# Kernel tuning notes

Measured on AMD Instinct MI355X. Metric: run time of the kernel, lower is better.

The kernel has to match this reference:

```python
import jax, jax.numpy as jnp
import numpy as np

D_MODEL = 256
NUM_HEADS = 4
D_K = D_MODEL // NUM_HEADS
SCALE = float(np.sqrt(D_K))


def setup_inputs() -> dict:
    key = jax.random.key(0)
    ks = jax.random.split(key, 11)
    B, S, D = 8, 2048, D_MODEL
    inp = {
        "query": jax.random.normal(ks[0], (B, S, D), dtype=jnp.float32),
        "key": jax.random.normal(ks[1], (B, S, D), dtype=jnp.float32),
        "value": jax.random.normal(ks[2], (B, S, D), dtype=jnp.float32),
        "W_q": jax.random.normal(ks[3], (D, D), dtype=jnp.float32) / np.sqrt(D),
        "b_q": jnp.zeros((D,), dtype=jnp.float32),
        "W_k": jax.random.normal(ks[4], (D, D), dtype=jnp.float32) / np.sqrt(D),
        "b_k": jnp.zeros((D,), dtype=jnp.float32),
        "W_v": jax.random.normal(ks[5], (D, D), dtype=jnp.float32) / np.sqrt(D),
        "b_v": jnp.zeros((D,), dtype=jnp.float32),
        "W_o": jax.random.normal(ks[6], (D, D), dtype=jnp.float32) / np.sqrt(D),
        "b_o": jnp.zeros((D,), dtype=jnp.float32),
    }
    return inp


def reference(query, key, value, W_q, b_q, W_k, b_k, W_v, b_v, W_o, b_o):
    B, Sq, D = query.shape
    Sk = key.shape[1]
    H, dk = NUM_HEADS, D_K
    # projections (torch Linear equivalent: x @ W + b with W as (in,out))
    Q = (query @ W_q + b_q).reshape(B, Sq, H, dk).transpose(0, 2, 1, 3)  # (B,H,Sq,dk)
    K = (key @ W_k + b_k).reshape(B, Sk, H, dk).transpose(0, 2, 1, 3)    # (B,H,Sk,dk)
    V = value @ W_v + b_v                                                # (B,Sk,D) shared across heads
    scores = jnp.einsum("bhqd,bhkd->bhqk", Q, K) / SCALE                 # (B,H,Sq,Sk)
    attn = jax.nn.softmax(scores, axis=-1)
    avg_attn = attn.mean(axis=1)                                         # (B,Sq,Sk)
    out = jnp.einsum("bqk,bkd->bqd", avg_attn, V)
    out = out @ W_o + b_o
    return out, avg_attn
```

## Files before the change

kernel.cpp:

```cpp
#include <hip/hip_runtime.h>
#include <stdint.h>

#define S2048 2048
#define DMODEL 256
#define NH 4
#define DK 64

typedef __bf16 bf16x8 __attribute__((ext_vector_type(8)));
typedef float f32x4 __attribute__((ext_vector_type(4)));

#define MFMA16(a, b, c) __builtin_amdgcn_mfma_f32_16x16x32_bf16((a), (b), (c), 0, 0, 0)

__device__ __forceinline__ uint16_t f2bf(float f) {
  uint32_t u = __builtin_bit_cast(uint32_t, f);
  u = (u + 0x7fff + ((u >> 16) & 1)) >> 16;
  return (uint16_t)u;
}

__device__ __forceinline__ void async16(const void* g, void* l) {
  __builtin_amdgcn_global_load_lds(
      (const __attribute__((address_space(1))) unsigned int*)g,
      (__attribute__((address_space(3))) unsigned int*)l, 16, 0, 0);
}

__device__ __forceinline__ void stage64(const char* gbase, int rstride,
                                        char* lds, int tid, int rows) {
  int iters = rows >> 5;
#pragma unroll
  for (int it = 0; it < iters; ++it) {
    int cid = (it << 8) + tid;
    int m = cid >> 3, cp = cid & 7, c = cp ^ (m & 7);
    async16(gbase + (size_t)m * rstride + (c << 4),
            lds + ((size_t)((it << 8) + (tid & ~63)) << 4));
  }
}

__device__ __forceinline__ bf16x8 frag_ld(const char* t, int rowbase, int chunk, int l15) {
  int m = rowbase + l15;
  return *(const bf16x8*)(t + (((m << 3) + (chunk ^ (m & 7))) << 4));
}

__global__ __launch_bounds__(256) void cast_x(const float* __restrict__ q,
                                              const float* __restrict__ k,
                                              const float* __restrict__ v,
                                              uint16_t* __restrict__ xq,
                                              uint16_t* __restrict__ xk,
                                              uint16_t* __restrict__ xv) {
  const float* src = blockIdx.y == 0 ? q : (blockIdx.y == 1 ? k : v);
  uint16_t* dst = blockIdx.y == 0 ? xq : (blockIdx.y == 1 ? xk : xv);
  size_t i = ((size_t)blockIdx.x * 256 + threadIdx.x) * 8;
  float4 a = *(const float4*)(src + i);
  float4 b = *(const float4*)(src + i + 4);
  union { uint16_t s[8]; uint4 u; } r;
  r.s[0] = f2bf(a.x); r.s[1] = f2bf(a.y); r.s[2] = f2bf(a.z); r.s[3] = f2bf(a.w);
  r.s[4] = f2bf(b.x); r.s[5] = f2bf(b.y); r.s[6] = f2bf(b.z); r.s[7] = f2bf(b.w);
  *(uint4*)(dst + i) = r.u;
}

__global__ __launch_bounds__(256) void cast_w(const float* __restrict__ Wq,
                                              const float* __restrict__ Wk,
                                              const float* __restrict__ Wv,
                                              const float* __restrict__ Wo,
                                              uint16_t* __restrict__ Wqt,
                                              uint16_t* __restrict__ Wkt,
                                              uint16_t* __restrict__ Wvt,
                                              uint16_t* __restrict__ Wot) {
  const float* W = blockIdx.y == 0 ? Wq : blockIdx.y == 1 ? Wk : blockIdx.y == 2 ? Wv : Wo;
  uint16_t* Wt = blockIdx.y == 0 ? Wqt : blockIdx.y == 1 ? Wkt : blockIdx.y == 2 ? Wvt : Wot;
  __shared__ uint16_t t[64 * 66];
  int tile = blockIdx.x, tr = tile >> 2, tc = tile & 3;
  int tid = threadIdx.x;
#pragma unroll
  for (int i = 0; i < 16; ++i) {
    int e = i * 256 + tid, r = e >> 6, cl = e & 63;
    t[r * 66 + cl] = f2bf(W[(size_t)(tr * 64 + r) * 256 + tc * 64 + cl]);
  }
  __syncthreads();
#pragma unroll
  for (int i = 0; i < 16; ++i) {
    int e = i * 256 + tid, n = e >> 6, kk = e & 63;
    Wt[(size_t)(tc * 64 + n) * 256 + tr * 64 + kk] = t[kk * 66 + n];
  }
}

template <int OUTF32, int BIAS>
__global__ __launch_bounds__(256) void gemm_bt(const uint16_t* __restrict__ A,
                                               const uint16_t* __restrict__ Bt,
                                               const float* __restrict__ bias,
                                               void* __restrict__ Cv, int K, int ldc) {
  __shared__ char lds[32768];
  char* At = lds;
  char* Btl = lds + 16384;
  int tid = threadIdx.x, lane = tid & 63, wid = tid >> 6;
  int l15 = lane & 15, q = lane >> 4;
  int mt = blockIdx.x, nt = blockIdx.y;
  int wm = (wid >> 1) * 64, wn = (wid & 1) * 64;
  f32x4 acc[4][4] = {};
  const char* Ag = (const char*)(A + (size_t)(mt * 128) * K);
  const char* Bg = (const char*)(Bt + (size_t)(nt * 128) * K);
  int nk = K >> 6;
  for (int kt = 0; kt < nk; ++kt) {
    stage64(Ag + kt * 128, K * 2, At, tid, 128);
    stage64(Bg + kt * 128, K * 2, Btl, tid, 128);
    __syncthreads();
#pragma unroll
    for (int ks = 0; ks < 2; ++ks) {
      bf16x8 a[4], b[4];
#pragma unroll
      for (int i = 0; i < 4; ++i) a[i] = frag_ld(At, wm + i * 16, ks * 4 + q, l15);
#pragma unroll
      for (int j = 0; j < 4; ++j) b[j] = frag_ld(Btl, wn + j * 16, ks * 4 + q, l15);
#pragma unroll
      for (int i = 0; i < 4; ++i)
#pragma unroll
        for (int j = 0; j < 4; ++j) acc[i][j] = MFMA16(a[i], b[j], acc[i][j]);
    }
    __syncthreads();
  }
#pragma unroll
  for (int i = 0; i < 4; ++i) {
    int r0 = mt * 128 + wm + i * 16 + q * 4;
#pragma unroll
    for (int j = 0; j < 4; ++j) {
      int c = nt * 128 + wn + j * 16 + l15;
#pragma unroll
      for (int e = 0; e < 4; ++e) {
        float v = acc[i][j][e];
        if (BIAS == 1) v += bias[c];
        if (BIAS == 2) v += bias[r0 + e];
        size_t off = (size_t)(r0 + e) * ldc + c;
        if (OUTF32) ((float*)Cv)[off] = v;
        else ((uint16_t*)Cv)[off] = f2bf(v);
      }
    }
  }
}

__global__ __launch_bounds__(256) void attn_lsum(const uint16_t* __restrict__ Qb,
                                                 const uint16_t* __restrict__ Kb,
                                                 float* __restrict__ linv4) {
  __shared__ char lds[32768];
  char* Qt = lds;
  char* Kt = lds + 16384;
  int tid = threadIdx.x, lane = tid & 63, wid = tid >> 6;
  int l15 = lane & 15, q = lane >> 4;
  int b = blockIdx.z, h = blockIdx.y, qt = blockIdx.x;
  const char* Qg = (const char*)(Qb + ((size_t)b * S2048 + qt * 128) * DMODEL + h * DK);
  const char* Kg = (const char*)(Kb + ((size_t)b * S2048) * DMODEL + h * DK);
  stage64(Qg, DMODEL * 2, Qt, tid, 128);
  float ps[2][4] = {};
  for (int kt = 0; kt < 16; ++kt) {
    stage64(Kg + (size_t)kt * 128 * (DMODEL * 2), DMODEL * 2, Kt, tid, 128);
    __syncthreads();
#pragma unroll
    for (int i = 0; i < 2; ++i) {
      bf16x8 a0 = frag_ld(Qt, wid * 32 + i * 16, q, l15);
      bf16x8 a1 = frag_ld(Qt, wid * 32 + i * 16, 4 + q, l15);
#pragma unroll
      for (int j = 0; j < 8; ++j) {
        f32x4 s = {0.f, 0.f, 0.f, 0.f};
        s = MFMA16(a0, frag_ld(Kt, j * 16, q, l15), s);
        s = MFMA16(a1, frag_ld(Kt, j * 16, 4 + q, l15), s);
#pragma unroll
        for (int e = 0; e < 4; ++e) ps[i][e] += __expf(s[e] * 0.125f);
      }
    }
    __syncthreads();
  }
#pragma unroll
  for (int i = 0; i < 2; ++i)
#pragma unroll
    for (int e = 0; e < 4; ++e) {
      float v = ps[i][e];
      v += __shfl_xor(v, 1); v += __shfl_xor(v, 2);
      v += __shfl_xor(v, 4); v += __shfl_xor(v, 8);
      if (l15 == 0) {
        int row = qt * 128 + wid * 32 + i * 16 + q * 4 + e;
        linv4[((size_t)(b * NH + h)) * S2048 + row] = 0.25f / v;
      }
    }
}

__global__ __launch_bounds__(256) void attn_avg(const uint16_t* __restrict__ Qb,
                                                const uint16_t* __restrict__ Kb,
                                                const float* __restrict__ linv4,
                                                float* __restrict__ attn) {
  __shared__ char lds[65536];
  char* Qt = lds;
  int tid = threadIdx.x, lane = tid & 63, wid = tid >> 6;
  int l15 = lane & 15, q = lane >> 4;
  int b = blockIdx.z, qt = blockIdx.y, kslice = blockIdx.x;
  size_t qrow0 = (size_t)b * S2048 + qt * 64;
#pragma unroll
  for (int h = 0; h < NH; ++h)
    stage64((const char*)(Qb + qrow0 * DMODEL + h * DK), DMODEL * 2, Qt + h * 8192, tid, 64);
  float li[4][4];
#pragma unroll
  for (int h = 0; h < NH; ++h)
#pragma unroll
    for (int e = 0; e < 4; ++e)
      li[h][e] = linv4[((size_t)(b * NH + h)) * S2048 + qt * 64 + wid * 16 + q * 4 + e];
  const char* Kg = (const char*)(Kb + ((size_t)b * S2048 + kslice * 512) * DMODEL);
  stage64(Kg, DMODEL * 2, lds + 32768, tid, 128);
  f32x4 Pav[8] = {};
  __syncthreads();
  for (int s = 0; s < 16; ++s) {
    int kt = s >> 2, h = s & 3;
    if (s + 1 < 16) {
      int kt2 = (s + 1) >> 2, h2 = (s + 1) & 3;
      stage64(Kg + (size_t)kt2 * 128 * (DMODEL * 2) + h2 * 128, DMODEL * 2,
              lds + 32768 + (((s + 1) & 1) << 14), tid, 128);
    }
    const char* Kc = lds + 32768 + ((s & 1) << 14);
    const char* Qh = Qt + h * 8192;
    bf16x8 a0 = frag_ld(Qh, wid * 16, q, l15);
    bf16x8 a1 = frag_ld(Qh, wid * 16, 4 + q, l15);
#pragma unroll
    for (int j = 0; j < 8; ++j) {
      f32x4 sA = {0.f, 0.f, 0.f, 0.f};
      sA = MFMA16(a0, frag_ld(Kc, j * 16, q, l15), sA);
      sA = MFMA16(a1, frag_ld(Kc, j * 16, 4 + q, l15), sA);
#pragma unroll
      for (int e = 0; e < 4; ++e) Pav[j][e] += __expf(sA[e] * 0.125f) * li[h][e];
    }
    if (h == 3) {
      size_t rowb = qrow0 + wid * 16 + q * 4;
      int colb = kslice * 512 + kt * 128 + l15;
#pragma unroll
      for (int j = 0; j < 8; ++j) {
#pragma unroll
        for (int e = 0; e < 4; ++e) {
          attn[(rowb + e) * S2048 + colb + j * 16] = Pav[j][e];
          Pav[j][e] = 0.f;
        }
      }
    }
    __syncthreads();
  }
}

__global__ __launch_bounds__(256) void pv_gemm(const float* __restrict__ attn,
                                               const uint16_t* __restrict__ VbT,
                                               uint16_t* __restrict__ out1) {
  __shared__ char lds[32768];
  char* At = lds;
  char* Btl = lds + 16384;
  int tid = threadIdx.x, lane = tid & 63, wid = tid >> 6;
  int l15 = lane & 15, q = lane >> 4;
  int mt = blockIdx.x, nt = blockIdx.y, b = blockIdx.z;
  int wm = (wid >> 1) * 64, wn = (wid & 1) * 64;
  f32x4 acc[4][4] = {};
  const float* Ag = attn + ((size_t)b * S2048 + mt * 128) * S2048;
  const char* Bg = (const char*)(VbT + (size_t)(nt * 128) * 16384 + (size_t)b * S2048);
  for (int kt = 0; kt < 32; ++kt) {
#pragma unroll
    for (int it = 0; it < 4; ++it) {
      int cid = it * 256 + tid;
      int m = cid >> 3, cp = cid & 7, c = cp ^ (m & 7);
      const float* src = Ag + (size_t)m * S2048 + kt * 64 + c * 8;
      float4 f0 = *(const float4*)src;
      float4 f1 = *(const float4*)(src + 4);
      union { uint16_t s[8]; uint4 u; } r;
      r.s[0] = f2bf(f0.x); r.s[1] = f2bf(f0.y); r.s[2] = f2bf(f0.z); r.s[3] = f2bf(f0.w);
      r.s[4] = f2bf(f1.x); r.s[5] = f2bf(f1.y); r.s[6] = f2bf(f1.z); r.s[7] = f2bf(f1.w);
      *(uint4*)(At + (size_t)cid * 16) = r.u;
    }
    stage64(Bg + kt * 128, 16384 * 2, Btl, tid, 128);
    __syncthreads();
#pragma unroll
    for (int ks = 0; ks < 2; ++ks) {
      bf16x8 a[4], bb[4];
#pragma unroll
      for (int i = 0; i < 4; ++i) a[i] = frag_ld(At, wm + i * 16, ks * 4 + q, l15);
#pragma unroll
      for (int j = 0; j < 4; ++j) bb[j] = frag_ld(Btl, wn + j * 16, ks * 4 + q, l15);
#pragma unroll
      for (int i = 0; i < 4; ++i)
#pragma unroll
        for (int j = 0; j < 4; ++j) acc[i][j] = MFMA16(a[i], bb[j], acc[i][j]);
    }
    __syncthreads();
  }
#pragma unroll
  for (int i = 0; i < 4; ++i) {
    size_t r0 = (size_t)b * S2048 + mt * 128 + wm + i * 16 + q * 4;
#pragma unroll
    for (int j = 0; j < 4; ++j) {
      int c = nt * 128 + wn + j * 16 + l15;
#pragma unroll
      for (int e = 0; e < 4; ++e) out1[(r0 + e) * DMODEL + c] = f2bf(acc[i][j][e]);
    }
  }
}

extern "C" void kernel_launch(void* const* d_in, const int* in_sizes, int n_in,
                              void* d_out, int out_size, void* d_ws, size_t ws_size,
                              hipStream_t stream) {
  const float* query = (const float*)d_in[0];
  const float* key_i = (const float*)d_in[1];
  const float* value = (const float*)d_in[2];
  const float* W_q = (const float*)d_in[3];
  const float* b_q = (const float*)d_in[4];
  const float* W_k = (const float*)d_in[5];
  const float* b_k = (const float*)d_in[6];
  const float* W_v = (const float*)d_in[7];
  const float* b_v = (const float*)d_in[8];
  const float* W_o = (const float*)d_in[9];
  const float* b_o = (const float*)d_in[10];

  char* ws = (char*)d_ws;
  const size_t SZX = 16384ull * 256 * 2;
  uint16_t* Xq = (uint16_t*)(ws + 0 * SZX);
  uint16_t* Xk = (uint16_t*)(ws + 1 * SZX);
  uint16_t* Xv = (uint16_t*)(ws + 2 * SZX);
  uint16_t* Qb = (uint16_t*)(ws + 3 * SZX);
  uint16_t* Kb = (uint16_t*)(ws + 4 * SZX);
  uint16_t* VbT = (uint16_t*)(ws + 5 * SZX);
  uint16_t* out1b = (uint16_t*)(ws + 6 * SZX);
  uint16_t* Wqt = (uint16_t*)(ws + 7 * SZX);
  uint16_t* Wkt = (uint16_t*)(ws + 7 * SZX + 131072);
  uint16_t* Wvt = (uint16_t*)(ws + 7 * SZX + 2 * 131072);
  uint16_t* Wot = (uint16_t*)(ws + 7 * SZX + 3 * 131072);
  float* linv4 = (float*)(ws + 7 * SZX + 4 * 131072);

  float* out = (float*)d_out;
  float* attn = out + 16384ull * 256;

  cast_x<<<dim3(2048, 3), 256, 0, stream>>>(query, key_i, value, Xq, Xk, Xv);
  cast_w<<<dim3(16, 4), 256, 0, stream>>>(W_q, W_k, W_v, W_o, Wqt, Wkt, Wvt, Wot);
  gemm_bt<0, 1><<<dim3(128, 2), 256, 0, stream>>>(Xq, Wqt, b_q, Qb, 256, 256);
  gemm_bt<0, 1><<<dim3(128, 2), 256, 0, stream>>>(Xk, Wkt, b_k, Kb, 256, 256);
  gemm_bt<0, 2><<<dim3(2, 128), 256, 0, stream>>>(Wvt, Xv, b_v, VbT, 256, 16384);
  attn_lsum<<<dim3(16, 4, 8), 256, 0, stream>>>(Qb, Kb, linv4);
  attn_avg<<<dim3(4, 32, 8), 256, 0, stream>>>(Qb, Kb, linv4, attn);
  pv_gemm<<<dim3(16, 2, 8), 256, 0, stream>>>(attn, VbT, out1b);
  gemm_bt<1, 1><<<dim3(128, 2), 256, 0, stream>>>(out1b, Wot, b_o, out, 256, 256);
}
```

Measured before the change: 366.0 us.

## Fuse averaged-attention computation with PV GEMM into one kernel

Replaces the separate attn_avg and pv_gemm kernels with one attn_fused kernel. Each block handles 32 query rows of one batch, computes the head-averaged probabilities per 32-key tile, writes them to the attn output, and multiplies them immediately against a staged V tile from LDS. This avoids re-reading the 128MB fp32 attn matrix and re-converting it to bf16. The cost is smaller per-block tiles, two barriers per key step, and only 512 blocks, which may limit occupancy and MFMA utilization.

```diff
diff --git a/kernel.cpp b/kernel.cpp
--- a/kernel.cpp
+++ b/kernel.cpp
@@ -38,6 +38,11 @@
 __device__ __forceinline__ bf16x8 frag_ld(const char* t, int rowbase, int chunk, int l15) {
   int m = rowbase + l15;
   return *(const bf16x8*)(t + (((m << 3) + (chunk ^ (m & 7))) << 4));
+}
+
+__device__ __forceinline__ bf16x8 frag_ld32(const char* t, int rowbase, int chunk, int l15) {
+  int m = rowbase + l15;
+  return *(const bf16x8*)(t + (((m << 2) + (chunk ^ (m & 3))) << 4));
 }
 
 __global__ __launch_bounds__(256) void cast_x(const float* __restrict__ q,
@@ -181,115 +186,97 @@
     }
 }
 
-__global__ __launch_bounds__(256) void attn_avg(const uint16_t* __restrict__ Qb,
-                                                const uint16_t* __restrict__ Kb,
-                                                const float* __restrict__ linv4,
-                                                float* __restrict__ attn) {
-  __shared__ char lds[65536];
-  char* Qt = lds;
+__global__ __launch_bounds__(256) void attn_fused(const uint16_t* __restrict__ Qb,
+                                                  const uint16_t* __restrict__ Kb,
+                                                  const uint16_t* __restrict__ VbT,
+                                                  const float* __restrict__ linv4,
+                                                  float* __restrict__ attn,
+                                                  uint16_t* __restrict__ out1) {
+  __shared__ __align__(16) char lds[51200];
+  char* Kt = lds;
+  char* Vt = lds + 16384;
+  char* Pt = lds + 49152;
   int tid = threadIdx.x, lane = tid & 63, wid = tid >> 6;
-  int l15 = lane & 15, q = lane >> 4;
-  int b = blockIdx.z, qt = blockIdx.y, kslice = blockIdx.x;
-  size_t qrow0 = (size_t)b * S2048 + qt * 64;
+  int l15 = lane & 15, hi = lane >> 4;
+  int b = blockIdx.x & 7, qt = blockIdx.x >> 3;
+  int qbase = qt * 32;
+  int wq = wid & 1, wk = wid >> 1;
+  int qg = wid & 1, dg = wid >> 1;
+  const char* Qg = (const char*)(Qb + ((size_t)b * S2048 + qbase) * DMODEL);
+  const char* Kg = (const char*)(Kb + (size_t)b * S2048 * DMODEL);
+  const char* Vgb = (const char*)(VbT + (size_t)b * S2048);
 #pragma unroll
   for (int h = 0; h < NH; ++h)
-    stage64((const char*)(Qb + qrow0 * DMODEL + h * DK), DMODEL * 2, Qt + h * 8192, tid, 64);
-  float li[4][4];
+    stage64(Qg + h * 128, DMODEL * 2, Kt + h * 4096, tid, 32);
+  float li[NH][4];
 #pragma unroll
   for (int h = 0; h < NH; ++h)
 #pragma unroll
     for (int e = 0; e < 4; ++e)
-      li[h][e] = linv4[((size_t)(b * NH + h)) * S2048 + qt * 64 + wid * 16 + q * 4 + e];
-  const char* Kg = (const char*)(Kb + ((size_t)b * S2048 + kslice * 512) * DMODEL);
-  stage64(Kg, DMODEL * 2, lds + 32768, tid, 128);
-  f32x4 Pav[8] = {};
+      li[h][e] = linv4[((size_t)(b * NH + h)) * S2048 + qbase + wq * 16 + hi * 4 + e];
   __syncthreads();
-  for (int s = 0; s < 16; ++s) {
-    int kt = s >> 2, h = s & 3;
-    if (s + 1 < 16) {
-      int kt2 = (s + 1) >> 2, h2 = (s + 1) & 3;
-      stage64(Kg + (size_t)kt2 * 128 * (DMODEL * 2) + h2 * 128, DMODEL * 2,
-              lds + 32768 + (((s + 1) & 1) << 14), tid, 128);
-    }
-    const char* Kc = lds + 32768 + ((s & 1) << 14);
-    const char* Qh = Qt + h * 8192;
-    bf16x8 a0 = frag_ld(Qh, wid * 16, q, l15);
-    bf16x8 a1 = frag_ld(Qh, wid * 16, 4 + q, l15);
-#pragma unroll
-    for (int j = 0; j < 8; ++j) {
-      f32x4 sA = {0.f, 0.f, 0.f, 0.f};
-      sA = MFMA16(a0, frag_ld(Kc, j * 16, q, l15), sA);
-      sA = MFMA16(a1, frag_ld(Kc, j * 16, 4 + q, l15), sA);
-#pragma unroll
-      for (int e = 0; e < 4; ++e) Pav[j][e] += __expf(sA[e] * 0.125f) * li[h][e];
-    }
-    if (h == 3) {
-      size_t rowb = qrow0 + wid * 16 + q * 4;
-      int colb = kslice * 512 + kt * 128 + l15;
+  bf16x8 qf[NH][2];
+#pragma unroll
+  for (int h = 0; h < NH; ++h)
+#pragma unroll
+    for (int ks = 0; ks < 2; ++ks)
+      qf[h][ks] = frag_ld(Kt + h * 4096, wq * 16, ks * 4 + hi, l15);
+  __syncthreads();
+#pragma unroll
+  for (int h = 0; h < NH; ++h)
+    stage64(Kg + h * 128, DMODEL * 2, Kt + h * 4096, tid, 32);
+  stage64(Vgb, 32768, Vt, tid, 256);
+  __syncthreads();
+  f32x4 acc[8] = {};
+  size_t arow0 = (size_t)b * S2048 + qbase + wq * 16 + hi * 4;
+#pragma unroll 2
+  for (int kt = 0; kt < 64; ++kt) {
+    float Pav[4] = {0.f, 0.f, 0.f, 0.f};
+#pragma unroll
+    for (int h = 0; h < NH; ++h) {
+      f32x4 s = {0.f, 0.f, 0.f, 0.f};
+      s = MFMA16(qf[h][0], frag_ld(Kt + h * 4096, wk * 16, hi, l15), s);
+      s = MFMA16(qf[h][1], frag_ld(Kt + h * 4096, wk * 16, 4 + hi, l15), s);
+#pragma unroll
+      for (int e = 0; e < 4; ++e) Pav[e] += __expf(s[e] * 0.125f) * li[h][e];
+    }
+#pragma unroll
+    for (int e = 0; e < 4; ++e) {
+      int m = wq * 16 + hi * 4 + e, kk = wk * 16 + l15;
+      *(uint16_t*)(Pt + (((m << 2) + ((kk >> 3) ^ (m & 3))) << 4) + ((kk & 7) << 1)) =
+          f2bf(Pav[e]);
+    }
+    __syncthreads();
+    {
+      int kc = kt * 32 + wk * 16 + l15;
+#pragma unroll
+      for (int e = 0; e < 4; ++e) attn[(arow0 + e) * S2048 + kc] = Pav[e];
+    }
+    if (kt + 1 < 64) {
+#pragma unroll
+      for (int h = 0; h < NH; ++h)
+        stage64(Kg + (size_t)(kt + 1) * 32 * (DMODEL * 2) + h * 128, DMODEL * 2,
+                Kt + h * 4096, tid, 32);
+    }
+    {
+      int ks = kt & 1;
+      bf16x8 pa = frag_ld32(Pt, qg * 16, hi, l15);
 #pragma unroll
       for (int j = 0; j < 8; ++j) {
-#pragma unroll
-        for (int e = 0; e < 4; ++e) {
-          attn[(rowb + e) * S2048 + colb + j * 16] = Pav[j][e];
-          Pav[j][e] = 0.f;
-        }
+        bf16x8 vb = frag_ld(Vt, dg * 128 + j * 16, ks * 4 + hi, l15);
+        acc[j] = MFMA16(pa, vb, acc[j]);
       }
     }
     __syncthreads();
-  }
-}
-
-__global__ __launch_bounds__(256) void pv_gemm(const float* __restrict__ attn,
-                                               const uint16_t* __restrict__ VbT,
-                                               uint16_t* __restrict__ out1) {
-  __shared__ char lds[32768];
-  char* At = lds;
-  char* Btl = lds + 16384;
-  int tid = threadIdx.x, lane = tid & 63, wid = tid >> 6;
-  int l15 = lane & 15, q = lane >> 4;
-  int mt = blockIdx.x, nt = blockIdx.y, b = blockIdx.z;
-  int wm = (wid >> 1) * 64, wn = (wid & 1) * 64;
-  f32x4 acc[4][4] = {};
-  const float* Ag = attn + ((size_t)b * S2048 + mt * 128) * S2048;
-  const char* Bg = (const char*)(VbT + (size_t)(nt * 128) * 16384 + (size_t)b * S2048);
-  for (int kt = 0; kt < 32; ++kt) {
-#pragma unroll
-    for (int it = 0; it < 4; ++it) {
-      int cid = it * 256 + tid;
-      int m = cid >> 3, cp = cid & 7, c = cp ^ (m & 7);
-      const float* src = Ag + (size_t)m * S2048 + kt * 64 + c * 8;
-      float4 f0 = *(const float4*)src;
-      float4 f1 = *(const float4*)(src + 4);
-      union { uint16_t s[8]; uint4 u; } r;
-      r.s[0] = f2bf(f0.x); r.s[1] = f2bf(f0.y); r.s[2] = f2bf(f0.z); r.s[3] = f2bf(f0.w);
-      r.s[4] = f2bf(f1.x); r.s[5] = f2bf(f1.y); r.s[6] = f2bf(f1.z); r.s[7] = f2bf(f1.w);
-      *(uint4*)(At + (size_t)cid * 16) = r.u;
-    }
-    stage64(Bg + kt * 128, 16384 * 2, Btl, tid, 128);
-    __syncthreads();
-#pragma unroll
-    for (int ks = 0; ks < 2; ++ks) {
-      bf16x8 a[4], bb[4];
-#pragma unroll
-      for (int i = 0; i < 4; ++i) a[i] = frag_ld(At, wm + i * 16, ks * 4 + q, l15);
-#pragma unroll
-      for (int j = 0; j < 4; ++j) bb[j] = frag_ld(Btl, wn + j * 16, ks * 4 + q, l15);
-#pragma unroll
-      for (int i = 0; i < 4; ++i)
-#pragma unroll
-        for (int j = 0; j < 4; ++j) acc[i][j] = MFMA16(a[i], bb[j], acc[i][j]);
-    }
-    __syncthreads();
-  }
-#pragma unroll
-  for (int i = 0; i < 4; ++i) {
-    size_t r0 = (size_t)b * S2048 + mt * 128 + wm + i * 16 + q * 4;
-#pragma unroll
-    for (int j = 0; j < 4; ++j) {
-      int c = nt * 128 + wn + j * 16 + l15;
-#pragma unroll
-      for (int e = 0; e < 4; ++e) out1[(r0 + e) * DMODEL + c] = f2bf(acc[i][j][e]);
-    }
+    if ((kt & 1) && kt + 1 < 64)
+      stage64(Vgb + (size_t)((kt + 1) >> 1) * 128, 32768, Vt, tid, 256);
+  }
+#pragma unroll
+  for (int j = 0; j < 8; ++j) {
+    size_t r0 = (size_t)b * S2048 + qbase + qg * 16 + hi * 4;
+    int c = dg * 128 + j * 16 + l15;
+#pragma unroll
+    for (int e = 0; e < 4; ++e) out1[(r0 + e) * DMODEL + c] = f2bf(acc[j][e]);
   }
 }
 
@@ -332,7 +319,6 @@
   gemm_bt<0, 1><<<dim3(128, 2), 256, 0, stream>>>(Xk, Wkt, b_k, Kb, 256, 256);
   gemm_bt<0, 2><<<dim3(2, 128), 256, 0, stream>>>(Wvt, Xv, b_v, VbT, 256, 16384);
   attn_lsum<<<dim3(16, 4, 8), 256, 0, stream>>>(Qb, Kb, linv4);
-  attn_avg<<<dim3(4, 32, 8), 256, 0, stream>>>(Qb, Kb, linv4, attn);
-  pv_gemm<<<dim3(16, 2, 8), 256, 0, stream>>>(attn, VbT, out1b);
+  attn_fused<<<dim3(512), 256, 0, stream>>>(Qb, Kb, VbT, linv4, attn, out1b);
   gemm_bt<1, 1><<<dim3(128, 2), 256, 0, stream>>>(out1b, Wot, b_o, out, 256, 256);
 }
```

Measured after the change: 343.4 us. -6.2%, faster.
